# Kernel tuning notes

Hardware: AMD Instinct MI355X
Metric: run time of the kernel (lower is better)

## Reference

```python
import jax, jax.numpy as jnp
import numpy as np

H_OUT, W_OUT = 473, 473  # original image size the logits are upsampled to
BN_EPS = 1e-5


def _conv(x, w, pad):
    return jax.lax.conv_general_dilated(
        x, w, window_strides=(1, 1), padding=[(pad, pad), (pad, pad)],
        dimension_numbers=('NCHW', 'OIHW', 'NCHW'))


def _bn(x, g, b):
    # BatchNorm2d in training mode: batch statistics over (N, H, W)
    m = jnp.mean(x, axis=(0, 2, 3), keepdims=True)
    v = jnp.var(x, axis=(0, 2, 3), keepdims=True)
    return (x - m) * jax.lax.rsqrt(v + BN_EPS) * g.reshape(1, -1, 1, 1) + b.reshape(1, -1, 1, 1)


def setup_inputs() -> dict:
    key = jax.random.key(0)
    ks = jax.random.split(key, 8)
    B, C, Hf, Wf, NC = 2, 256, 60, 60, 2
    return {
        'V_a': jax.random.normal(ks[0], (B, C, Hf, Wf), jnp.float32),
        'V_b': jax.random.normal(ks[1], (B, C, Hf, Wf), jnp.float32),
        'D_a': jax.random.normal(ks[2], (B, C, Hf, Wf), jnp.float32),
        'W_e': jax.random.normal(ks[3], (C, C), jnp.float32) * 0.02,
        'gate_w': jax.random.normal(ks[4], (1, C, 1, 1), jnp.float32) * 0.01,
        'conv1_w': jax.random.normal(ks[5], (C, 3 * C, 3, 3), jnp.float32) * 0.01,
        'conv2_w': jax.random.normal(ks[6], (C, 2 * C, 3, 3), jnp.float32) * 0.01,
        'bn1_g': jnp.ones((C,), jnp.float32),
        'bn1_b': jnp.zeros((C,), jnp.float32),
        'bn2_g': jnp.ones((C,), jnp.float32),
        'bn2_b': jnp.zeros((C,), jnp.float32),
        'cls1_w': jax.random.normal(ks[7], (NC, C, 1, 1), jnp.float32) * 0.01,
        'cls1_b': jnp.zeros((NC,), jnp.float32),
        'cls2_w': jax.random.normal(jax.random.fold_in(key, 9), (NC, C, 1, 1), jnp.float32) * 0.01,
        'cls2_b': jnp.zeros((NC,), jnp.float32),
    }


def reference(V_a, V_b, D_a, W_e, gate_w, conv1_w, conv2_w,
              bn1_g, bn1_b, bn2_g, bn2_b, cls1_w, cls1_b, cls2_w, cls2_b):
    B, C, Hf, Wf = V_a.shape
    N = Hf * Wf
    V_a_flat = V_a.reshape(B, C, N)
    V_b_flat = V_b.reshape(B, C, N)

    # linear_e on transposed A features, then affinity S = (A^T W^T) B
    weighted = jnp.einsum('bcn,dc->bnd', V_a_flat, W_e)        # [B, N, C]
    S = jnp.einsum('bnd,bdm->bnm', weighted, V_b_flat)         # [B, N, N]

    S_row = jax.nn.softmax(S, axis=1)                          # softmax over dim 1
    S_colT = jax.nn.softmax(jnp.swapaxes(S, 1, 2), axis=1)     # softmax of S^T over dim 1

    Z_b = jnp.einsum('bcn,bnm->bcm', V_a_flat, S_row)          # attended for view b
    Z_a = jnp.einsum('bcn,bnm->bcm', V_b_flat, S_colT)         # attended for view a

    att1 = Z_a.reshape(B, C, Hf, Wf)
    att2 = Z_b.reshape(B, C, Hf, Wf)

    # 1x1 sigmoid gates
    att1 = att1 * jax.nn.sigmoid(_conv(att1, gate_w, 0))
    att2 = att2 * jax.nn.sigmoid(_conv(att2, gate_w, 0))

    # conc1: branch-1 concatenates gated attention, RGB feat, and depth feat
    x1 = jnp.concatenate([att1, V_a, D_a], axis=1)             # [B, 3C, Hf, Wf]
    x2 = jnp.concatenate([att2, V_b], axis=1)                  # [B, 2C, Hf, Wf]

    x1 = jax.nn.relu(_bn(_conv(x1, conv1_w, 1), bn1_g, bn1_b))
    x2 = jax.nn.relu(_bn(_conv(x2, conv2_w, 1), bn2_g, bn2_b))

    x1 = _conv(x1, cls1_w, 0) + cls1_b.reshape(1, -1, 1, 1)
    x2 = _conv(x2, cls2_w, 0) + cls2_b.reshape(1, -1, 1, 1)

    NC = cls1_w.shape[0]
    x1 = jax.image.resize(x1, (B, NC, H_OUT, W_OUT), 'linear')
    x2 = jax.image.resize(x2, (B, NC, H_OUT, W_OUT), 'linear')
    return jax.nn.sigmoid(x1), jax.nn.sigmoid(x2)
```

## Files before the change

### kernel.cpp

```cpp
#include <hip/hip_runtime.h>

#define BB 2
#define CC 256
#define NN 3600
#define NCH 2
#define HO 473
#define WO 473
#define NP 3648
#define NR 3712
#define NTI 29
#define ZKS 6
#define CZKS 3

typedef unsigned short u16;
typedef __attribute__((ext_vector_type(8))) short short8;
typedef __attribute__((ext_vector_type(4))) float f32x4;

static __device__ __forceinline__ u16 f2bf(float f) {
    unsigned u = __float_as_uint(f);
    unsigned r = (u + 0x7FFF + ((u >> 16) & 1)) >> 16;
    return (u16)r;
}
static __device__ __forceinline__ u16 f2h(float f) {
    _Float16 h = (_Float16)f;
    return __builtin_bit_cast(unsigned short, h);
}
static __device__ __forceinline__ float h2f(u16 u) {
    _Float16 h = __builtin_bit_cast(_Float16, u);
    return (float)h;
}

static __device__ __forceinline__ void glds16(const u16* g, u16* l) {
    __builtin_amdgcn_global_load_lds(
        (const __attribute__((address_space(1))) void*)g,
        (__attribute__((address_space(3))) void*)l, 16, 0, 0);
}


__global__ __launch_bounds__(256)
void gemm_we(const u16* __restrict__ vat, const u16* __restrict__ web,
             u16* __restrict__ wgtb)
{
    __shared__ u16 As[128 * 64];
    __shared__ u16 Bs[128 * 64];
    const u16* A = vat + (long)blockIdx.z * NR * CC;
    u16* Cp = wgtb + (long)blockIdx.z * NR * CC;

    const int t = threadIdx.x;
    const int w = t >> 6, lane = t & 63;
    const int mh = (w >> 1) * 64, nh = (w & 1) * 64;
    const int lm = lane & 15, quad = lane >> 4;
    const int m0 = blockIdx.y * 128, n0 = blockIdx.x * 128;
    const int wb = t & 192;

    f32x4 acc[4][4] = {};

    for (int k0 = 0; k0 < CC; k0 += 64) {
#pragma unroll
        for (int i = 0; i < 4; ++i) {
            int idx = i * 256 + t;
            int row = idx >> 3;
            int sc8 = ((idx ^ row) & 7) * 8;
            glds16(A + (long)(m0 + row) * CC + k0 + sc8, &As[(i * 256 + wb) * 8]);
            glds16(web + (long)(n0 + row) * CC + k0 + sc8, &Bs[(i * 256 + wb) * 8]);
        }
        __syncthreads();
#pragma unroll
        for (int s = 0; s < 2; ++s) {
            short8 a[4], b[4];
#pragma unroll
            for (int i = 0; i < 4; ++i)
                a[i] = *(const short8*)(&As[(mh + i * 16 + lm) * 64 + ((s * 4 + quad) ^ (lm & 7)) * 8]);
#pragma unroll
            for (int j = 0; j < 4; ++j)
                b[j] = *(const short8*)(&Bs[(nh + j * 16 + lm) * 64 + ((s * 4 + quad) ^ (lm & 7)) * 8]);
#pragma unroll
            for (int i = 0; i < 4; ++i)
#pragma unroll
                for (int j = 0; j < 4; ++j)
                    acc[i][j] = __builtin_amdgcn_mfma_f32_16x16x32_bf16(a[i], b[j], acc[i][j], 0, 0, 0);
        }
        __syncthreads();
    }
#pragma unroll
    for (int i = 0; i < 4; ++i)
#pragma unroll
        for (int r = 0; r < 4; ++r) {
            int row = m0 + mh + i * 16 + quad * 4 + r;
            if (row < NN)
#pragma unroll
                for (int j = 0; j < 4; ++j) {
                    int col = n0 + nh + j * 16 + lm;
                    if (col < CC) Cp[(long)row * CC + col] = f2bf(acc[i][j][r]);
                }
        }
}

__global__ __launch_bounds__(256)
void gemm_s_stats(const u16* __restrict__ A, const u16* __restrict__ B,
                  u16* __restrict__ Sh, u16* __restrict__ STh,
                  float* __restrict__ prowm, float* __restrict__ prows,
                  float* __restrict__ pcolm, float* __restrict__ pcols)
{
    __shared__ u16 smem[17408];
    u16* As = smem;
    u16* Bs = smem + 8192;

    const int t = threadIdx.x;
    const int w = t >> 6, lane = t & 63;
    const int mh = (w >> 1) * 64, nh = (w & 1) * 64;
    const int lm = lane & 15, quad = lane >> 4;
    const int m0 = blockIdx.y * 128, n0 = blockIdx.x * 128;
    const int wb = t & 192;

    f32x4 acc[4][4] = {};

    for (int k0 = 0; k0 < CC; k0 += 64) {
#pragma unroll
        for (int i = 0; i < 4; ++i) {
            int idx = i * 256 + t;
            int row = idx >> 3;
            int sc8 = ((idx ^ row) & 7) * 8;
            glds16(A + (long)(m0 + row) * CC + k0 + sc8, &As[(i * 256 + wb) * 8]);
            glds16(B + (long)(n0 + row) * CC + k0 + sc8, &Bs[(i * 256 + wb) * 8]);
        }
        __syncthreads();
#pragma unroll
        for (int s = 0; s < 2; ++s) {
            short8 a[4], b[4];
#pragma unroll
            for (int i = 0; i < 4; ++i)
                a[i] = *(const short8*)(&As[(mh + i * 16 + lm) * 64 + ((s * 4 + quad) ^ (lm & 7)) * 8]);
#pragma unroll
            for (int j = 0; j < 4; ++j)
                b[j] = *(const short8*)(&Bs[(nh + j * 16 + lm) * 64 + ((s * 4 + quad) ^ (lm & 7)) * 8]);
#pragma unroll
            for (int i = 0; i < 4; ++i)
#pragma unroll
                for (int j = 0; j < 4; ++j)
                    acc[i][j] = __builtin_amdgcn_mfma_f32_16x16x32_bf16(a[i], b[j], acc[i][j], 0, 0, 0);
        }
        __syncthreads();
    }

    u16* tr = smem;

#pragma unroll
    for (int i = 0; i < 4; ++i)
#pragma unroll
        for (int j = 0; j < 4; ++j)
#pragma unroll
            for (int r = 0; r < 4; ++r)
                tr[(mh + i * 16 + quad * 4 + r) * 136 + (nh + j * 16 + lm)] = f2h(acc[i][j][r]);
    __syncthreads();
    {
        int row = t >> 1, hf = t & 1;
        int ng = m0 + row;
        if (ng < NN) {
#pragma unroll
            for (int q = 0; q < 8; ++q) {
                int cb = n0 + hf * 64 + q * 8;
                if (cb < NN)
                    *(uint4*)(&Sh[(long)ng * NP + cb]) =
                        *(const uint4*)(&tr[row * 136 + hf * 64 + q * 8]);
            }
        }
    }
    __syncthreads();

    bool cval[4];
#pragma unroll
    for (int j = 0; j < 4; ++j) cval[j] = (n0 + nh + j * 16 + lm) < NN;

    float* sm = (float*)smem;
    float* rowm = sm;
    float* rows_ = sm + 256;
    float* colm = sm + 512;
    float* cols_ = sm + 768;

#pragma unroll
    for (int i = 0; i < 4; ++i)
#pragma unroll
        for (int r = 0; r < 4; ++r) {
            float m = -3.0e38f;
#pragma unroll
            for (int j = 0; j < 4; ++j) if (cval[j]) m = fmaxf(m, acc[i][j][r]);
            m = fmaxf(m, __shfl_xor(m, 1, 64));
            m = fmaxf(m, __shfl_xor(m, 2, 64));
            m = fmaxf(m, __shfl_xor(m, 4, 64));
            m = fmaxf(m, __shfl_xor(m, 8, 64));
            float s = 0.f;
#pragma unroll
            for (int j = 0; j < 4; ++j) if (cval[j]) s += __expf(acc[i][j][r] - m);
            s += __shfl_xor(s, 1, 64);
            s += __shfl_xor(s, 2, 64);
            s += __shfl_xor(s, 4, 64);
            s += __shfl_xor(s, 8, 64);
            if (lm == 0) {
                int rr = mh + i * 16 + quad * 4 + r;
                rowm[(w & 1) * 128 + rr] = m;
                rows_[(w & 1) * 128 + rr] = s;
            }
        }

#pragma unroll
    for (int j = 0; j < 4; ++j) {
        float m = -3.0e38f;
#pragma unroll
        for (int i = 0; i < 4; ++i)
#pragma unroll
            for (int r = 0; r < 4; ++r)
                if (m0 + mh + i * 16 + quad * 4 + r < NN) m = fmaxf(m, acc[i][j][r]);
        m = fmaxf(m, __shfl_xor(m, 16, 64));
        m = fmaxf(m, __shfl_xor(m, 32, 64));
        float s = 0.f;
#pragma unroll
        for (int i = 0; i < 4; ++i)
#pragma unroll
            for (int r = 0; r < 4; ++r)
                if (m0 + mh + i * 16 + quad * 4 + r < NN) s += __expf(acc[i][j][r] - m);
        s += __shfl_xor(s, 16, 64);
        s += __shfl_xor(s, 32, 64);
        if (quad == 0) {
            int ccl = nh + j * 16 + lm;
            colm[(w >> 1) * 128 + ccl] = m;
            cols_[(w >> 1) * 128 + ccl] = s;
        }
    }
    __syncthreads();

    if (t < 128) {
        float m1 = rowm[t], m2 = rowm[128 + t];
        float M = fmaxf(m1, m2);
        float s = rows_[t] * __expf(m1 - M) + rows_[128 + t] * __expf(m2 - M);
        if (m0 + t < NN) {
            prowm[(long)blockIdx.x * NR + m0 + t] = M;
            prows[(long)blockIdx.x * NR + m0 + t] = s;
        }
    } else {
        int c = t - 128;
        float m1 = colm[c], m2 = colm[128 + c];
        float M = fmaxf(m1, m2);
        float s = cols_[c] * __expf(m1 - M) + cols_[128 + c] * __expf(m2 - M);
        if (n0 + c < NN) {
            pcolm[(long)blockIdx.y * NR + n0 + c] = M;
            pcols[(long)blockIdx.y * NR + n0 + c] = s;
        }
    }

    __syncthreads();
#pragma unroll
    for (int i = 0; i < 4; ++i)
#pragma unroll
        for (int j = 0; j < 4; ++j)
#pragma unroll
            for (int r = 0; r < 4; ++r)
                tr[(nh + j * 16 + lm) * 136 + (mh + i * 16 + quad * 4 + r)] = f2h(acc[i][j][r]);
    __syncthreads();
    {
        int row = t >> 1, hf = t & 1;
        int mg = n0 + row;
        if (mg < NN) {
#pragma unroll
            for (int q = 0; q < 8; ++q) {
                int cb = m0 + hf * 64 + q * 8;
                if (cb < NN)
                    *(uint4*)(&STh[(long)mg * NP + cb]) =
                        *(const uint4*)(&tr[row * 136 + hf * 64 + q * 8]);
            }
        }
    }
}

__global__ __launch_bounds__(256)
void stats_final(const float* __restrict__ prm, const float* __restrict__ prs,
                 const float* __restrict__ pcm, const float* __restrict__ pcs,
                 float* __restrict__ rm, float* __restrict__ ri,
                 float* __restrict__ cm, float* __restrict__ ci)
{
    int i = blockIdx.x * 256 + threadIdx.x;
    if (i >= NN) return;
    const float* pm = blockIdx.y ? pcm : prm;
    const float* ps = blockIdx.y ? pcs : prs;
    float m = -3.0e38f, s = 0.f;
#pragma unroll 4
    for (int tI = 0; tI < NTI; ++tI) {
        float m2 = pm[(long)tI * NR + i], s2 = ps[(long)tI * NR + i];
        float M = fmaxf(m, m2);
        s = s * __expf(m - M) + s2 * __expf(m2 - M);
        m = M;
    }
    float inv = 1.f / s;
    if (blockIdx.y) { cm[i] = m; ci[i] = inv; }
    else            { rm[i] = m; ri[i] = inv; }
}

__global__ __launch_bounds__(256, 4)
void gemm_z_128(const u16* __restrict__ vab_b, const u16* __restrict__ vbb_b,
                const u16* __restrict__ STh, const u16* __restrict__ Sh,
                const float* __restrict__ rm, const float* __restrict__ ri,
                const float* __restrict__ cm, const float* __restrict__ ci,
                float* __restrict__ Zb_b, float* __restrict__ Za_b)
{
    __shared__ u16 As[128 * 64];
    __shared__ u16 Bs[128 * 64];

    const int t = threadIdx.x;
    const int w = t >> 6, lane = t & 63;
    const int mh = (w >> 1) * 64, nh = (w & 1) * 64;
    const int lm = lane & 15, quad = lane >> 4;
    const int n0 = blockIdx.x * 128;
    const int ks = blockIdx.y;
    const int zz = blockIdx.z;
    const int branch = zz & 1;
    const int m0 = (zz >> 1) * 128;
    const u16* A = branch ? vbb_b : vab_b;
    const u16* B = branch ? Sh : STh;
    const float* mxp = branch ? rm : cm;
    const float* isp = branch ? ri : ci;
    float* Cp = branch ? Za_b : Zb_b;
    const int wb = t & 192;

    const int base = 57 / ZKS, rem = 57 % ZKS;
    const int it0 = ks * base + (ks < rem ? ks : rem);
    const int itn = base + (ks < rem ? 1 : 0);

    int rowv[4], sc8v[4];
    const u16* Brow[4];
    float bm[4], bi[4];
#pragma unroll
    for (int i = 0; i < 4; ++i) {
        int idx = i * 256 + t;
        int row = idx >> 3;
        rowv[i] = row;
        sc8v[i] = ((idx ^ row) & 7) * 8;
        int rg = n0 + row;
        int rc = rg < NN ? rg : 0;
        Brow[i] = B + (long)rg * NP + sc8v[i];
        bm[i] = mxp[rc];
        bi[i] = isp[rc];
    }

    f32x4 acc[4][4] = {};

    for (int it = it0; it < it0 + itn; ++it) {
        const int k0 = it * 64;
#pragma unroll
        for (int i = 0; i < 4; ++i)
            glds16(A + (long)(m0 + rowv[i]) * NP + k0 + sc8v[i], &As[(i * 256 + wb) * 8]);
#pragma unroll
        for (int i = 0; i < 4; ++i) {
            u16 o[8];
            if (k0 + sc8v[i] < NN) {
                uint4 v = *(const uint4*)(Brow[i] + k0);
                const u16* hp = (const u16*)&v;
#pragma unroll
                for (int e = 0; e < 8; ++e)
                    o[e] = f2bf(__expf(h2f(hp[e]) - bm[i]) * bi[i]);
            } else {
#pragma unroll
                for (int e = 0; e < 8; ++e) o[e] = 0;
            }
            *(uint4*)(&Bs[(i * 256 + t) * 8]) = *(const uint4*)o;
        }
        __syncthreads();
#pragma unroll
        for (int s = 0; s < 2; ++s) {
            short8 a[4], b[4];
#pragma unroll
            for (int i = 0; i < 4; ++i)
                a[i] = *(const short8*)(&As[(mh + i * 16 + lm) * 64 + ((s * 4 + quad) ^ (lm & 7)) * 8]);
#pragma unroll
            for (int j = 0; j < 4; ++j)
                b[j] = *(const short8*)(&Bs[(nh + j * 16 + lm) * 64 + ((s * 4 + quad) ^ (lm & 7)) * 8]);
#pragma unroll
            for (int i = 0; i < 4; ++i)
#pragma unroll
                for (int j = 0; j < 4; ++j)
                    acc[i][j] = __builtin_amdgcn_mfma_f32_16x16x32_bf16(a[i], b[j], acc[i][j], 0, 0, 0);
        }
        __syncthreads();
    }

#pragma unroll
    for (int i = 0; i < 4; ++i)
#pragma unroll
        for (int r = 0; r < 4; ++r) {
            int row = m0 + mh + i * 16 + quad * 4 + r;
#pragma unroll
            for (int j = 0; j < 4; ++j) {
                int col = n0 + nh + j * 16 + lm;
                if (col < NN)
                    atomicAdd(&Cp[(long)row * NN + col], acc[i][j][r]);
            }
        }
}

__global__ __launch_bounds__(256, 4)
void conv_both(const u16* __restrict__ W1, const u16* __restrict__ W2,
               const u16* __restrict__ gzaT, const u16* __restrict__ vat,
               const u16* __restrict__ daT, const u16* __restrict__ gzbT,
               const u16* __restrict__ vbt, const u16* __restrict__ zbuf,
               float* __restrict__ y1, float* __restrict__ y2)
{
    __shared__ u16 As[128 * 64];
    __shared__ u16 Bs[128 * 64];

    const int t = threadIdx.x;
    const int w = t >> 6, lane = t & 63;
    const int mh = (w >> 1) * 64, nh = (w & 1) * 64;
    const int lm = lane & 15, quad = lane >> 4;
    const int wb = t & 192;

    const long L = blockIdx.x + (long)NTI * (blockIdx.y + (long)CZKS * blockIdx.z);
    const int combo = (int)(L & 7);
    const long rest = L >> 3;
    const int ks = (int)(rest % CZKS);
    const int px = (int)(rest / CZKS);
    const int which = combo >> 2;
    const int b = (combo >> 1) & 1;
    const int m0 = (combo & 1) * 128;
    const int n0 = px * 128;

    const int CIN = which ? 512 : 768;
    const int KT = 9 * CIN;
    const u16* W = which ? W2 : W1;
    const u16* P0 = which ? gzbT : gzaT;
    const u16* P1 = which ? vbt : vat;
    const u16* P2 = which ? vbt : daT;
    float* Y = which ? y2 : y1;
    const long pstride = (long)NR * CC;

    const int PER = 3 * (CIN / 64);
    const int it0 = ks * PER;
    const int dh = ks - 1;

    int rowv[4], sc8v[4], rb[4];
    bool okd[4][3];
#pragma unroll
    for (int i = 0; i < 4; ++i) {
        int idx = i * 256 + t;
        int row = idx >> 3;
        rowv[i] = row;
        sc8v[i] = ((idx ^ row) & 7) * 8;
        int pq = n0 + row;
        int h = pq / 60, wp = pq - h * 60;
        rb[i] = (pq + dh * 60) * CC + sc8v[i];
        bool hok = (pq < NN) && ((unsigned)(h + dh) < 60u);
#pragma unroll
        for (int d = 0; d < 3; ++d)
            okd[i][d] = hok && ((unsigned)(wp + d - 1) < 60u);
    }

    f32x4 acc[4][4] = {};

    for (int it = it0; it < it0 + PER; ++it) {
        const int k0 = it * 64;
        const int g = it - it0;
        const int dw = g % 3;
        const int pc = g / 3;
        const int plane = pc >> 2;
        const int cip = (pc & 3) * 64;
        const u16* srcp = ((plane == 0) ? P0 : (plane == 1) ? P1 : P2)
                          + (long)b * pstride + cip;

#pragma unroll
        for (int i = 0; i < 4; ++i) {
            glds16(W + (long)(m0 + rowv[i]) * KT + k0 + sc8v[i], &As[(i * 256 + wb) * 8]);
            const u16* gs = okd[i][dw] ? srcp + rb[i] + (dw - 1) * CC : zbuf;
            glds16(gs, &Bs[(i * 256 + wb) * 8]);
        }
        __syncthreads();
#pragma unroll
        for (int s = 0; s < 2; ++s) {
            short8 a[4], bfr[4];
#pragma unroll
            for (int i = 0; i < 4; ++i)
                a[i] = *(const short8*)(&As[(mh + i * 16 + lm) * 64 + ((s * 4 + quad) ^ (lm & 7)) * 8]);
#pragma unroll
            for (int j = 0; j < 4; ++j)
                bfr[j] = *(const short8*)(&Bs[(nh + j * 16 + lm) * 64 + ((s * 4 + quad) ^ (lm & 7)) * 8]);
#pragma unroll
            for (int i = 0; i < 4; ++i)
#pragma unroll
                for (int j = 0; j < 4; ++j)
                    acc[i][j] = __builtin_amdgcn_mfma_f32_16x16x32_bf16(a[i], bfr[j], acc[i][j], 0, 0, 0);
        }
        __syncthreads();
    }

    float* out = Y + (long)b * CC * NN;
#pragma unroll
    for (int i = 0; i < 4; ++i)
#pragma unroll
        for (int r = 0; r < 4; ++r) {
            int row = m0 + mh + i * 16 + quad * 4 + r;
#pragma unroll
            for (int j = 0; j < 4; ++j) {
                int col = n0 + nh + j * 16 + lm;
                if (col < NN)
                    atomicAdd(&out[(long)row * NN + col], acc[i][j][r]);
            }
        }
}

__global__ __launch_bounds__(256)
void cvt_we(const float* __restrict__ W, u16* __restrict__ O)
{
    int i = blockIdx.x * 256 + threadIdx.x;
    if (i < CC * CC) O[i] = f2bf(W[i]);
}

__global__ __launch_bounds__(256)
void transpose_cvt3(const float* __restrict__ Va, const float* __restrict__ Vb,
                    const float* __restrict__ Da,
                    u16* __restrict__ vat, u16* __restrict__ vbt,
                    u16* __restrict__ daT,
                    u16* __restrict__ vab, u16* __restrict__ vbb)
{
    __shared__ float tile[64][65];
    int z = blockIdx.z;
    int s = z % 3, b = z / 3;
    const float* V = (s == 0) ? Va : (s == 1) ? Vb : Da;
    u16* VT = (s == 0) ? vat : (s == 1) ? vbt : daT;
    u16* Vpad = (s == 0) ? vab : (s == 1) ? vbb : nullptr;

    int c0 = blockIdx.y * 64, n0 = blockIdx.x * 64;
    int t = threadIdx.x;
#pragma unroll
    for (int e = 0; e < 16; ++e) {
        int f = e * 256 + t; int i = f >> 6, j = f & 63;
        int n = n0 + j;
        float v = 0.f;
        if (n < NN) v = V[((long)b * CC + c0 + i) * NN + n];
        tile[i][j] = v;
        if (Vpad) Vpad[((long)b * CC + c0 + i) * NP + n] = f2bf(v);
    }
    __syncthreads();
#pragma unroll
    for (int e = 0; e < 16; ++e) {
        int f = e * 256 + t; int i = f >> 6, j = f & 63;
        int n = n0 + i;
        if (n < NN) VT[((long)b * NR + n) * CC + c0 + j] = f2bf(tile[j][i]);
    }
}

__global__ __launch_bounds__(256)
void transpose_gate(const float* __restrict__ Za, const float* __restrict__ Zb,
                    const float* __restrict__ sga, const float* __restrict__ sgb,
                    u16* __restrict__ gzaT, u16* __restrict__ gzbT)
{
    __shared__ float tile[64][65];
    int z = blockIdx.z;
    int b = z & 1, ab = z >> 1;
    const float* Z = ab ? Zb : Za;
    const float* sg = ab ? sgb : sga;
    u16* ZT = ab ? gzbT : gzaT;

    int c0 = blockIdx.y * 64, n0 = blockIdx.x * 64;
    int t = threadIdx.x;
#pragma unroll
    for (int e = 0; e < 16; ++e) {
        int f = e * 256 + t; int i = f >> 6, j = f & 63;
        int n = n0 + j;
        float v = 0.f;
        if (n < NN) v = Z[((long)b * CC + c0 + i) * NN + n];
        tile[i][j] = v;
    }
    __syncthreads();
#pragma unroll
    for (int e = 0; e < 16; ++e) {
        int f = e * 256 + t; int i = f >> 6, j = f & 63;
        int n = n0 + i;
        if (n < NN)
            ZT[((long)b * NR + n) * CC + c0 + j] = f2bf(tile[j][i] * sg[b * NN + n]);
    }
}

template<int CIN>
__global__ __launch_bounds__(256)
void cvt_convw(const float* __restrict__ W, u16* __restrict__ O)
{
    const int KT = 9 * CIN;
    const int PER = 3 * (CIN / 64);
    long idx = (long)blockIdx.x * 256 + threadIdx.x;
    if (idx >= (long)CC * KT) return;
    int co = (int)(idx / KT);
    int r = (int)(idx % KT);
    int c64 = r >> 6, within = r & 63;
    int ks = c64 / PER, g = c64 % PER;
    int dw = g % 3, pc = g / 3;
    int tap = ks * 3 + dw;
    int ci = pc * 64 + within;
    O[idx] = f2bf(W[((long)co * CIN + ci) * 9 + tap]);
}

__global__ __launch_bounds__(256)
void gate_sig(const float* __restrict__ Za, const float* __restrict__ Zb,
              const float* __restrict__ gw,
              float* __restrict__ sga, float* __restrict__ sgb)
{
    int t = threadIdx.x;
    int px = t & 63, ck = t >> 6;
    int b = blockIdx.y;
    int ab = blockIdx.z;
    const float* Z = ab ? Zb : Za;
    float* sg = ab ? sgb : sga;
    int p = blockIdx.x * 64 + px;
    const float* Zp = Z + (long)b * CC * NN;
    float g = 0.f;
    if (p < NN) {
        for (int c = ck * 64; c < ck * 64 + 64; ++c) g += gw[c] * Zp[(long)c * NN + p];
    }
    __shared__ float red[256];
    red[t] = g;
    __syncthreads();
    if (t < 64) {
        int pp = blockIdx.x * 64 + t;
        if (pp < NN) {
            float tot = red[t] + red[t + 64] + red[t + 128] + red[t + 192];
            sg[b * NN + pp] = 1.f / (1.f + __expf(-tot));
        }
    }
}

__global__ __launch_bounds__(256)
void bn_stats_kernel(const float* __restrict__ y1, const float* __restrict__ y2,
                     const float* __restrict__ g1, const float* __restrict__ b1,
                     const float* __restrict__ g2, const float* __restrict__ b2,
                     float* __restrict__ sc1, float* __restrict__ sh1,
                     float* __restrict__ sc2, float* __restrict__ sh2)
{
    int which = blockIdx.x >> 8;
    int c = blockIdx.x & 255, t = threadIdx.x;
    const float* Y = which ? y2 : y1;
    const float* g = which ? g2 : g1;
    const float* beta = which ? b2 : b1;
    float* scale = which ? sc2 : sc1;
    float* shift = which ? sh2 : sh1;
    float s = 0.f, sq = 0.f;
    for (int b = 0; b < BB; ++b) {
        const float* p = Y + (long)b * CC * NN + (long)c * NN;
        for (int i = t; i < NN; i += 256) { float v = p[i]; s += v; sq += v * v; }
    }
    __shared__ float ls[256], lq[256];
    ls[t] = s; lq[t] = sq;
    __syncthreads();
    for (int off = 128; off > 0; off >>= 1) {
        if (t < off) { ls[t] += ls[t + off]; lq[t] += lq[t + off]; }
        __syncthreads();
    }
    if (t == 0) {
        const float inv = 1.f / (float)(BB * NN);
        float mean = ls[0] * inv;
        float var = fmaxf(lq[0] * inv - mean * mean, 0.f);
        float sc = g[c] * rsqrtf(var + 1e-5f);
        scale[c] = sc;
        shift[c] = beta[c] - mean * sc;
    }
}

__global__ __launch_bounds__(256)
void cls_kernel(const float* __restrict__ y1, const float* __restrict__ y2,
                const float* __restrict__ sc1, const float* __restrict__ sh1,
                const float* __restrict__ sc2, const float* __restrict__ sh2,
                const float* __restrict__ cw1, const float* __restrict__ cb1,
                const float* __restrict__ cw2, const float* __restrict__ cb2,
                float* __restrict__ O1, float* __restrict__ O2)
{
    int which = blockIdx.z;
    const float* Y = which ? y2 : y1;
    const float* scale = which ? sc2 : sc1;
    const float* shift = which ? sh2 : sh1;
    const float* cw = which ? cw2 : cw1;
    const float* cb = which ? cb2 : cb1;
    float* O = which ? O2 : O1;

    int t = threadIdx.x;
    int px = t & 63, ck = t >> 6;
    int b = blockIdx.y;
    int p = blockIdx.x * 64 + px;
    const float* Yb = Y + (long)b * CC * NN;
    float a0 = 0.f, a1 = 0.f;
    if (p < NN) {
        for (int c = ck * 64; c < ck * 64 + 64; ++c) {
            float v = Yb[(long)c * NN + p] * scale[c] + shift[c];
            v = fmaxf(v, 0.f);
            a0 += cw[c] * v;
            a1 += cw[CC + c] * v;
        }
    }
    __shared__ float r0[256], r1[256];
    r0[t] = a0; r1[t] = a1;
    __syncthreads();
    if (t < 64) {
        int pp = blockIdx.x * 64 + t;
        if (pp < NN) {
            float s0 = r0[t] + r0[t + 64] + r0[t + 128] + r0[t + 192];
            float s1 = r1[t] + r1[t + 64] + r1[t + 128] + r1[t + 192];
            O[(long)b * NCH * NN + pp] = s0 + cb[0];
            O[(long)b * NCH * NN + NN + pp] = s1 + cb[1];
        }
    }
}

__global__ __launch_bounds__(256)
void resize_sig_kernel(const float* __restrict__ I1, const float* __restrict__ I2,
                       float* __restrict__ O)
{
    const long HALF = (long)BB * NCH * HO * WO;
    long gid = (long)blockIdx.x * 256 + threadIdx.x;
    if (gid >= HALF) return;
    int half = blockIdx.y;
    const float* I = half ? I2 : I1;
    float* Op = O + half * HALF;

    int j = (int)(gid % WO);
    long r = gid / WO;
    int i = (int)(r % HO);
    int pc = (int)(r / HO);
    const float* ip = I + (long)pc * NN;

    const float SCL = 60.0f / 473.0f;
    float fy = (i + 0.5f) * SCL - 0.5f;
    float fx = (j + 0.5f) * SCL - 0.5f;
    int y0 = (int)floorf(fy);
    int x0 = (int)floorf(fx);
    float ty = fy - (float)y0;
    float tx = fx - (float)x0;
    int y0c = max(y0, 0), y1c = min(y0 + 1, 59);
    int x0c = max(x0, 0), x1c = min(x0 + 1, 59);
    float va = ip[y0c * 60 + x0c], vb = ip[y0c * 60 + x1c];
    float vc = ip[y1c * 60 + x0c], vd = ip[y1c * 60 + x1c];
    float v = (1.f - ty) * ((1.f - tx) * va + tx * vb) + ty * ((1.f - tx) * vc + tx * vd);
    Op[gid] = 1.f / (1.f + __expf(-v));
}

extern "C" void kernel_launch(void* const* d_in, const int* in_sizes, int n_in,
                              void* d_out, int out_size, void* d_ws, size_t ws_size,
                              hipStream_t stream)
{
    const float* V_a    = (const float*)d_in[0];
    const float* V_b    = (const float*)d_in[1];
    const float* D_a    = (const float*)d_in[2];
    const float* W_e    = (const float*)d_in[3];
    const float* gate_w = (const float*)d_in[4];
    const float* conv1_w = (const float*)d_in[5];
    const float* conv2_w = (const float*)d_in[6];
    const float* bn1_g = (const float*)d_in[7];
    const float* bn1_b = (const float*)d_in[8];
    const float* bn2_g = (const float*)d_in[9];
    const float* bn2_b = (const float*)d_in[10];
    const float* cls1_w = (const float*)d_in[11];
    const float* cls1_b = (const float*)d_in[12];
    const float* cls2_w = (const float*)d_in[13];
    const float* cls2_b = (const float*)d_in[14];
    float* out = (float*)d_out;

    size_t off = 0;
    char* wsb = (char*)d_ws;
    auto carve = [&](size_t bytes) -> char* {
        char* p = wsb + off; off += (bytes + 255) & ~(size_t)255; return p;
    };

    u16* Sh    = (u16*)carve((size_t)NR * NP * 2);
    u16* STh   = (u16*)carve((size_t)NR * NP * 2);
    u16* vab   = (u16*)carve((size_t)BB * CC * NP * 2);
    u16* vbb   = (u16*)carve((size_t)BB * CC * NP * 2);
    u16* vat   = (u16*)carve((size_t)BB * NR * CC * 2);
    u16* vbt   = (u16*)carve((size_t)BB * NR * CC * 2);
    u16* daT   = (u16*)carve((size_t)BB * NR * CC * 2);
    u16* gzaT  = (u16*)carve((size_t)BB * NR * CC * 2);
    u16* gzbT  = (u16*)carve((size_t)BB * NR * CC * 2);
    u16* wgtb  = (u16*)carve((size_t)BB * NR * CC * 2);
    u16* zbuf  = (u16*)carve(256);
    u16* web   = (u16*)carve((size_t)CC * CC * 2);
    u16* wt1   = (u16*)carve((size_t)CC * 9 * 768 * 2);
    u16* wt2   = (u16*)carve((size_t)CC * 9 * 512 * 2);
    float* Za  = (float*)carve((size_t)BB * CC * NN * 4);
    float* Zb  = (float*)carve((size_t)BB * CC * NN * 4);
    float* y1  = (float*)carve((size_t)BB * CC * NN * 4);
    float* y2  = (float*)carve((size_t)BB * CC * NN * 4);
    float* rmx = (float*)carve((size_t)BB * NN * 4);
    float* rsm = (float*)carve((size_t)BB * NN * 4);
    float* cmx = (float*)carve((size_t)BB * NN * 4);
    float* csm = (float*)carve((size_t)BB * NN * 4);
    float* sga = (float*)carve((size_t)BB * NN * 4);
    float* sgb = (float*)carve((size_t)BB * NN * 4);
    float* prm = (float*)carve((size_t)NTI * NR * 4);
    float* prs = (float*)carve((size_t)NTI * NR * 4);
    float* pcm = (float*)carve((size_t)NTI * NR * 4);
    float* pcs = (float*)carve((size_t)NTI * NR * 4);
    float* c1o = (float*)carve((size_t)BB * NCH * NN * 4);
    float* c2o = (float*)carve((size_t)BB * NCH * NN * 4);

    dim3 blk(256);

    hipMemsetAsync(Za, 0, (size_t)4 * BB * CC * NN * 4, stream);
    hipMemsetAsync(zbuf, 0, 256, stream);

    cvt_we<<<256, blk, 0, stream>>>(W_e, web);
    transpose_cvt3<<<dim3(57, 4, 3 * BB), blk, 0, stream>>>(
        V_a, V_b, D_a, vat, vbt, daT, vab, vbb);
    cvt_convw<768><<<(int)(((long)CC * 9 * 768 + 255) / 256), blk, 0, stream>>>(conv1_w, wt1);
    cvt_convw<512><<<(int)(((long)CC * 9 * 512 + 255) / 256), blk, 0, stream>>>(conv2_w, wt2);

    gemm_we<<<dim3(2, NTI, BB), blk, 0, stream>>>(vat, web, wgtb);

    for (int b = 0; b < BB; ++b) {
        const u16* wgtb_b = wgtb + (long)b * NR * CC;
        const u16* vbt_b  = vbt + (long)b * NR * CC;
        const u16* vab_b  = vab + (long)b * CC * NP;
        const u16* vbb_b  = vbb + (long)b * CC * NP;
        float* rmx_b = rmx + b * NN; float* rsm_b = rsm + b * NN;
        float* cmx_b = cmx + b * NN; float* csm_b = csm + b * NN;

        gemm_s_stats<<<dim3(NTI, NTI), blk, 0, stream>>>(
            wgtb_b, vbt_b, Sh, STh, prm, prs, pcm, pcs);
        stats_final<<<dim3((NN + 255) / 256, 2), blk, 0, stream>>>(
            prm, prs, pcm, pcs, rmx_b, rsm_b, cmx_b, csm_b);
        gemm_z_128<<<dim3(NTI, ZKS, 4), blk, 0, stream>>>(
            vab_b, vbb_b, STh, Sh, rmx_b, rsm_b, cmx_b, csm_b,
            Zb + (long)b * CC * NN, Za + (long)b * CC * NN);
    }

    gate_sig<<<dim3(57, BB, 2), blk, 0, stream>>>(Za, Zb, gate_w, sga, sgb);
    transpose_gate<<<dim3(57, 4, 2 * BB), blk, 0, stream>>>(Za, Zb, sga, sgb, gzaT, gzbT);

    conv_both<<<dim3(NTI, CZKS, 8), blk, 0, stream>>>(
        wt1, wt2, gzaT, vat, daT, gzbT, vbt, zbuf, y1, y2);

    bn_stats_kernel<<<2 * CC, blk, 0, stream>>>(
        y1, y2, bn1_g, bn1_b, bn2_g, bn2_b, rmx, rsm, cmx, csm);
    cls_kernel<<<dim3(57, BB, 2), blk, 0, stream>>>(
        y1, y2, rmx, rsm, cmx, csm, cls1_w, cls1_b, cls2_w, cls2_b, c1o, c2o);

    resize_sig_kernel<<<dim3((int)(((long)BB * NCH * HO * WO + 255) / 256), 2), blk, 0, stream>>>(c1o, c2o, out);
}
```

Baseline: 593.6 us.

## Widen gemm_z K-tile to 128 and pad S buffers to NR stride

The attention-apply GEMM now loads a 128-wide K slice per iteration instead of 64, which halves the number of barrier-separated iterations and lets each load batch more work. The split-K factor drops from 6 to 4 and occupancy hints drop to 2 blocks per CU to fit the doubled shared memory. S, S^T and the padded V buffers switch to an NR row stride so that 128-wide K tiles stay in bounds, and B loads are now issued unconditionally with only the exp conversion guarded. The trade-off is fewer concurrent blocks and less split-K parallelism in exchange for fewer syncs and larger tiles.

```diff
diff --git a/kernel.cpp b/kernel.cpp
--- a/kernel.cpp
+++ b/kernel.cpp
@@ -6,10 +6,10 @@
 #define NCH 2
 #define HO 473
 #define WO 473
-#define NP 3648
 #define NR 3712
 #define NTI 29
-#define ZKS 6
+#define ZKI 29
+#define ZKS 4
 #define CZKS 3
 
 typedef unsigned short u16;
@@ -161,7 +161,7 @@
             for (int q = 0; q < 8; ++q) {
                 int cb = n0 + hf * 64 + q * 8;
                 if (cb < NN)
-                    *(uint4*)(&Sh[(long)ng * NP + cb]) =
+                    *(uint4*)(&Sh[(long)ng * NR + cb]) =
                         *(const uint4*)(&tr[row * 136 + hf * 64 + q * 8]);
             }
         }
@@ -265,7 +265,7 @@
             for (int q = 0; q < 8; ++q) {
                 int cb = m0 + hf * 64 + q * 8;
                 if (cb < NN)
-                    *(uint4*)(&STh[(long)mg * NP + cb]) =
+                    *(uint4*)(&STh[(long)mg * NR + cb]) =
                         *(const uint4*)(&tr[row * 136 + hf * 64 + q * 8]);
             }
         }
@@ -295,15 +295,15 @@
     else            { rm[i] = m; ri[i] = inv; }
 }
 
-__global__ __launch_bounds__(256, 4)
+__global__ __launch_bounds__(256, 2)
 void gemm_z_128(const u16* __restrict__ vab_b, const u16* __restrict__ vbb_b,
                 const u16* __restrict__ STh, const u16* __restrict__ Sh,
                 const float* __restrict__ rm, const float* __restrict__ ri,
                 const float* __restrict__ cm, const float* __restrict__ ci,
                 float* __restrict__ Zb_b, float* __restrict__ Za_b)
 {
-    __shared__ u16 As[128 * 64];
-    __shared__ u16 Bs[128 * 64];
+    __shared__ u16 As[128 * 128];
+    __shared__ u16 Bs[128 * 128];
 
     const int t = threadIdx.x;
     const int w = t >> 6, lane = t & 63;
@@ -321,22 +321,23 @@
     float* Cp = branch ? Za_b : Zb_b;
     const int wb = t & 192;
 
-    const int base = 57 / ZKS, rem = 57 % ZKS;
+    const int base = ZKI / ZKS, rem = ZKI % ZKS;
     const int it0 = ks * base + (ks < rem ? ks : rem);
     const int itn = base + (ks < rem ? 1 : 0);
 
-    int rowv[4], sc8v[4];
-    const u16* Brow[4];
-    float bm[4], bi[4];
-#pragma unroll
-    for (int i = 0; i < 4; ++i) {
+    int scv[8];
+    const u16* Arow[8];
+    const u16* Brow[8];
+    float bm[8], bi[8];
+#pragma unroll
+    for (int i = 0; i < 8; ++i) {
         int idx = i * 256 + t;
-        int row = idx >> 3;
-        rowv[i] = row;
-        sc8v[i] = ((idx ^ row) & 7) * 8;
+        int row = idx >> 4, c = idx & 15;
+        scv[i] = (c & 8) * 8 + ((c ^ row) & 7) * 8;
+        Arow[i] = A + (long)(m0 + row) * NR + scv[i];
         int rg = n0 + row;
+        Brow[i] = B + (long)rg * NR + scv[i];
         int rc = rg < NN ? rg : 0;
-        Brow[i] = B + (long)rg * NP + sc8v[i];
         bm[i] = mxp[rc];
         bi[i] = isp[rc];
     }
@@ -344,16 +345,16 @@
     f32x4 acc[4][4] = {};
 
     for (int it = it0; it < it0 + itn; ++it) {
-        const int k0 = it * 64;
-#pragma unroll
-        for (int i = 0; i < 4; ++i)
-            glds16(A + (long)(m0 + rowv[i]) * NP + k0 + sc8v[i], &As[(i * 256 + wb) * 8]);
-#pragma unroll
-        for (int i = 0; i < 4; ++i) {
+        const int k0 = it * 128;
+#pragma unroll
+        for (int i = 0; i < 8; ++i)
+            glds16(Arow[i] + k0, &As[(i * 256 + wb) * 8]);
+#pragma unroll
+        for (int i = 0; i < 8; ++i) {
             u16 o[8];
-            if (k0 + sc8v[i] < NN) {
-                uint4 v = *(const uint4*)(Brow[i] + k0);
-                const u16* hp = (const u16*)&v;
+            uint4 v = *(const uint4*)(Brow[i] + k0);
+            const u16* hp = (const u16*)&v;
+            if (k0 + scv[i] < NN) {
 #pragma unroll
                 for (int e = 0; e < 8; ++e)
                     o[e] = f2bf(__expf(h2f(hp[e]) - bm[i]) * bi[i]);
@@ -365,14 +366,15 @@
         }
         __syncthreads();
 #pragma unroll
-        for (int s = 0; s < 2; ++s) {
+        for (int s = 0; s < 4; ++s) {
+            const int sl = ((s >> 1) * 8 + (((s & 1) * 4 + quad) ^ (lm & 7))) * 8;
             short8 a[4], b[4];
 #pragma unroll
             for (int i = 0; i < 4; ++i)
-                a[i] = *(const short8*)(&As[(mh + i * 16 + lm) * 64 + ((s * 4 + quad) ^ (lm & 7)) * 8]);
+                a[i] = *(const short8*)(&As[(mh + i * 16 + lm) * 128 + sl]);
 #pragma unroll
             for (int j = 0; j < 4; ++j)
-                b[j] = *(const short8*)(&Bs[(nh + j * 16 + lm) * 64 + ((s * 4 + quad) ^ (lm & 7)) * 8]);
+                b[j] = *(const short8*)(&Bs[(nh + j * 16 + lm) * 128 + sl]);
 #pragma unroll
             for (int i = 0; i < 4; ++i)
 #pragma unroll
@@ -534,7 +536,7 @@
         float v = 0.f;
         if (n < NN) v = V[((long)b * CC + c0 + i) * NN + n];
         tile[i][j] = v;
-        if (Vpad) Vpad[((long)b * CC + c0 + i) * NP + n] = f2bf(v);
+        if (Vpad) Vpad[((long)b * CC + c0 + i) * NR + n] = f2bf(v);
     }
     __syncthreads();
 #pragma unroll
@@ -763,10 +765,10 @@
         char* p = wsb + off; off += (bytes + 255) & ~(size_t)255; return p;
     };
 
-    u16* Sh    = (u16*)carve((size_t)NR * NP * 2);
-    u16* STh   = (u16*)carve((size_t)NR * NP * 2);
-    u16* vab   = (u16*)carve((size_t)BB * CC * NP * 2);
-    u16* vbb   = (u16*)carve((size_t)BB * CC * NP * 2);
+    u16* Sh    = (u16*)carve((size_t)NR * NR * 2);
+    u16* STh   = (u16*)carve((size_t)NR * NR * 2);
+    u16* vab   = (u16*)carve((size_t)BB * CC * NR * 2);
+    u16* vbb   = (u16*)carve((size_t)BB * CC * NR * 2);
     u16* vat   = (u16*)carve((size_t)BB * NR * CC * 2);
     u16* vbt   = (u16*)carve((size_t)BB * NR * CC * 2);
     u16* daT   = (u16*)carve((size_t)BB * NR * CC * 2);
@@ -800,7 +802,7 @@
     hipMemsetAsync(zbuf, 0, 256, stream);
 
     cvt_we<<<256, blk, 0, stream>>>(W_e, web);
-    transpose_cvt3<<<dim3(57, 4, 3 * BB), blk, 0, stream>>>(
+    transpose_cvt3<<<dim3(58, 4, 3 * BB), blk, 0, stream>>>(
         V_a, V_b, D_a, vat, vbt, daT, vab, vbb);
     cvt_convw<768><<<(int)(((long)CC * 9 * 768 + 255) / 256), blk, 0, stream>>>(conv1_w, wt1);
     cvt_convw<512><<<(int)(((long)CC * 9 * 512 + 255) / 256), blk, 0, stream>>>(conv2_w, wt2);
@@ -810,8 +812,8 @@
     for (int b = 0; b < BB; ++b) {
         const u16* wgtb_b = wgtb + (long)b * NR * CC;
         const u16* vbt_b  = vbt + (long)b * NR * CC;
-        const u16* vab_b  = vab + (long)b * CC * NP;
-        const u16* vbb_b  = vbb + (long)b * CC * NP;
+        const u16* vab_b  = vab + (long)b * CC * NR;
+        const u16* vbb_b  = vbb + (long)b * CC * NR;
         float* rmx_b = rmx + b * NN; float* rsm_b = rsm + b * NN;
         float* cmx_b = cmx + b * NN; float* csm_b = csm + b * NN;
 
```

New measurement: 547.1 us. 7.8% less time.
